# Optimization experiments

Hardware: AMD Instinct MI355X
Metric: run time of the kernel (lower is better)

Reference implementation:

```python
import jax, jax.numpy as jnp
import numpy as np

NEG_SLOPE = 0.01  # torch F.leaky_relu default
EPS = 1e-12


def setup_inputs() -> dict:
    key = jax.random.key(0)
    k1, k2, k3, k4 = jax.random.split(key, 4)
    num_nodes, in_f, out_f, num_edges = 50000, 128, 128, 600000
    x = jax.random.normal(k1, (num_nodes, in_f), dtype=jnp.float32)
    edge_index = jax.random.randint(k2, (2, num_edges), 0, num_nodes, dtype=jnp.int64)
    # xavier_uniform for W:[out,in]
    limit = float(np.sqrt(6.0 / (in_f + out_f)))
    W = jax.random.uniform(k3, (out_f, in_f), dtype=jnp.float32, minval=-limit, maxval=limit)
    a = jax.random.uniform(k4, (2 * out_f,), dtype=jnp.float32, minval=0.0, maxval=1.0)
    return {"x": x, "edge_index": edge_index, "W": W, "a": a}


def reference(x, edge_index, W, a):
    num_nodes = x.shape[0]
    out_f = W.shape[0]
    # add self loops
    loops = jnp.arange(num_nodes, dtype=edge_index.dtype)
    src = jnp.concatenate([edge_index[0], loops])
    dst = jnp.concatenate([edge_index[1], loops])
    messages = x @ W.T                      # [N, F_out]
    # cat([h_src,h_dst]) @ a == h_src @ a[:F] + h_dst @ a[F:] (avoids materializing concat)
    s_src = messages @ a[:out_f]            # [N]
    s_dst = messages @ a[out_f:]            # [N]
    e_ij = jax.nn.leaky_relu(s_src[src] + s_dst[dst], negative_slope=NEG_SLOPE)  # [E]
    w = jnp.exp(e_ij)                       # unnormalized edge weights
    denom = jax.ops.segment_sum(w, dst, num_segments=num_nodes)
    denom = jnp.maximum(denom, EPS)
    weighted = w[:, None] * messages[src]   # [E, F_out]
    agg = jax.ops.segment_sum(weighted, dst, num_segments=num_nodes)
    return agg / denom[:, None]
```

## Files before the change

### kernel.cpp

```cpp
#include <hip/hip_runtime.h>

#define NEG_SLOPE 0.01f
#define CH 4096
#define BSHIFT 9
#define BINW 512
#define NBMAX 128

typedef __attribute__((ext_vector_type(8))) short bf16x8;
typedef __attribute__((ext_vector_type(4))) float f32x4;

static __device__ __forceinline__ unsigned short f2bf(float f) {
  unsigned u = __float_as_uint(f);
  u += 0x7fffu + ((u >> 16) & 1u);
  return (unsigned short)(u >> 16);
}

__global__ __launch_bounds__(256) void k_setup(const float* __restrict__ W,
                                               const float* __restrict__ a,
                                               unsigned short* __restrict__ Wb,
                                               float* __restrict__ p_lo,
                                               float* __restrict__ p_hi,
                                               int* __restrict__ bin_cursor) {
  int b = blockIdx.x;
  int t = threadIdx.x;
  if (b < 64) {
    int i = b * 256 + t;
    Wb[i] = f2bf(W[i]);
    if (b == 0 && t < NBMAX) bin_cursor[t] = 0;
  } else {
    if (t < 128) {
      float lo = 0.f, hi = 0.f;
#pragma unroll 8
      for (int f = 0; f < 128; ++f) {
        float w = W[f * 128 + t];
        lo += w * a[f];
        hi += w * a[128 + f];
      }
      p_lo[t] = lo;
      p_hi[t] = hi;
    }
  }
}

__global__ __launch_bounds__(256) void k_work(const float* __restrict__ x,
                                              const float* __restrict__ p_lo,
                                              const float* __restrict__ p_hi,
                                              const unsigned short* __restrict__ Wb,
                                              unsigned short* __restrict__ msgs,
                                              float* __restrict__ s_src,
                                              float* __restrict__ s_dst, int N,
                                              const int* __restrict__ ei,
                                              int* __restrict__ bin_cursor,
                                              int2* __restrict__ binbuf, int E,
                                              int SB, int BINCAP) {
  __shared__ int hist[NBMAX], base[NBMAX], cur[NBMAX], gbase[NBMAX];
  __shared__ int2 stage[CH];
  int t = threadIdx.x;
  if ((int)blockIdx.x < SB) {
    int e0 = blockIdx.x * CH;
    int cntE = E - e0; if (cntE > CH) cntE = CH;
    if (t < NBMAX) { hist[t] = 0; cur[t] = 0; }
    __syncthreads();
    int srcs[CH / 256], dsts[CH / 256];
#pragma unroll
    for (int j = 0; j < CH / 256; ++j) {
      int i = t + j * 256;
      if (i < cntE) {
        srcs[j] = ei[e0 + i];
        dsts[j] = ei[E + e0 + i];
        atomicAdd(&hist[dsts[j] >> BSHIFT], 1);
      }
    }
    __syncthreads();
    if (t < NBMAX) base[t] = hist[t];
    __syncthreads();
    for (int d = 1; d < NBMAX; d <<= 1) {
      int v = (t < NBMAX && t >= d) ? base[t - d] : 0;
      __syncthreads();
      if (t < NBMAX) base[t] += v;
      __syncthreads();
    }
    if (t < NBMAX) {
      base[t] -= hist[t];
      gbase[t] = hist[t] ? atomicAdd(&bin_cursor[t], hist[t]) : 0;
    }
    __syncthreads();
#pragma unroll
    for (int j = 0; j < CH / 256; ++j) {
      int i = t + j * 256;
      if (i < cntE) {
        int bin = dsts[j] >> BSHIFT;
        int p = base[bin] + atomicAdd(&cur[bin], 1);
        stage[p] = make_int2(srcs[j], dsts[j]);
      }
    }
    __syncthreads();
    for (int i = t; i < cntE; i += 256) {
      int2 ed = stage[i];
      int bin = ed.y >> BSHIFT;
      int idx = gbase[bin] + (i - base[bin]);
      if (idx < BINCAP) binbuf[(size_t)bin * BINCAP + idx] = ed;
    }
    return;
  }
  int bb = blockIdx.x - SB;
  int wave = (bb * 256 + t) >> 6;
  int lane = t & 63;
  int baseN = wave * 16;
  if (baseN >= N) return;
  int q = lane >> 4, r = lane & 15;
  int node = baseN + r;
  const float* xrow = x + (size_t)node * 128 + q * 8;
  const float4* pl = (const float4*)p_lo;
  const float4* ph = (const float4*)p_hi;
  bf16x8 afrag[4];
  float lo = 0.f, hi = 0.f;
#pragma unroll
  for (int c = 0; c < 4; ++c) {
    float4 v0 = *(const float4*)(xrow + c * 32);
    float4 v1 = *(const float4*)(xrow + c * 32 + 4);
    int fi = q * 2 + c * 8;
    float4 a0 = pl[fi], a1 = pl[fi + 1];
    float4 b0 = ph[fi], b1 = ph[fi + 1];
    lo += v0.x * a0.x + v0.y * a0.y + v0.z * a0.z + v0.w * a0.w
        + v1.x * a1.x + v1.y * a1.y + v1.z * a1.z + v1.w * a1.w;
    hi += v0.x * b0.x + v0.y * b0.y + v0.z * b0.z + v0.w * b0.w
        + v1.x * b1.x + v1.y * b1.y + v1.z * b1.z + v1.w * b1.w;
    bf16x8 f;
    f[0] = (short)f2bf(v0.x); f[1] = (short)f2bf(v0.y);
    f[2] = (short)f2bf(v0.z); f[3] = (short)f2bf(v0.w);
    f[4] = (short)f2bf(v1.x); f[5] = (short)f2bf(v1.y);
    f[6] = (short)f2bf(v1.z); f[7] = (short)f2bf(v1.w);
    afrag[c] = f;
  }
  lo += __shfl_xor(lo, 16); lo += __shfl_xor(lo, 32);
  hi += __shfl_xor(hi, 16); hi += __shfl_xor(hi, 32);
  if (q == 0) { s_src[node] = lo; s_dst[node] = hi; }
#pragma unroll
  for (int ft = 0; ft < 8; ++ft) {
    const unsigned short* wrow = Wb + (size_t)(ft * 16 + r) * 128 + q * 8;
    f32x4 acc = {0.f, 0.f, 0.f, 0.f};
#pragma unroll
    for (int c = 0; c < 4; ++c) {
      bf16x8 bfrag = *(const bf16x8*)(wrow + c * 32);
      acc = __builtin_amdgcn_mfma_f32_16x16x32_bf16(afrag[c], bfrag, acc, 0, 0, 0);
    }
#pragma unroll
    for (int rr = 0; rr < 4; ++rr) {
      int n2 = baseN + q * 4 + rr;
      msgs[(size_t)n2 * 128 + ft * 16 + r] = f2bf(acc[rr]);
    }
  }
}

__global__ __launch_bounds__(256) void k_pass2(const int2* __restrict__ binbuf,
                                               const int* __restrict__ bin_cursor,
                                               unsigned* __restrict__ csr,
                                               int2* __restrict__ meta,
                                               int N, int BINCAP) {
  __shared__ int hist[BINW], scanv[BINW], cur[BINW];
  __shared__ int tmp[256];
  int b = blockIdx.x, t = threadIdx.x;
  int cnt = bin_cursor[b]; if (cnt > BINCAP) cnt = BINCAP;
  const int2* bb = binbuf + (size_t)b * BINCAP;
  hist[t] = 0; hist[t + 256] = 0;
  __syncthreads();
  for (int i = t; i < cnt; i += 256)
    atomicAdd(&hist[bb[i].y & (BINW - 1)], 1);
  __syncthreads();
  int v0 = hist[2 * t], v1 = hist[2 * t + 1];
  tmp[t] = v0 + v1;
  __syncthreads();
  for (int d = 1; d < 256; d <<= 1) {
    int v = (t >= d) ? tmp[t - d] : 0;
    __syncthreads();
    tmp[t] += v;
    __syncthreads();
  }
  int excl = tmp[t] - (v0 + v1);
  scanv[2 * t] = excl;
  scanv[2 * t + 1] = excl + v0;
  cur[2 * t] = 0; cur[2 * t + 1] = 0;
  __syncthreads();
  int gb = b * BINCAP;
  for (int l = t; l < BINW; l += 256) {
    int dst = b * BINW + l;
    if (dst < N) meta[dst] = make_int2(gb + scanv[l], hist[l]);
  }
  __syncthreads();
  for (int i = t; i < cnt; i += 256) {
    int2 ed = bb[i];
    int l = ed.y & (BINW - 1);
    int p = atomicAdd(&cur[l], 1);
    csr[gb + scanv[l] + p] = (unsigned)ed.x;
  }
}

__global__ __launch_bounds__(256) void k_agg(const unsigned short* __restrict__ msgs,
                                             const int2* __restrict__ meta,
                                             const unsigned* __restrict__ csr,
                                             const float* __restrict__ s_src,
                                             const float* __restrict__ s_dst,
                                             float* __restrict__ out, int N) {
  int wave = (blockIdx.x * 256 + threadIdx.x) >> 6;
  int lane = threadIdx.x & 63;
  if (wave >= N) return;
  int node = wave;
  int g = lane >> 4;
  int r = lane & 15;
  float sdn = s_dst[node];
  float zs = s_src[node] + sdn;
  zs = zs > 0.f ? zs : NEG_SLOPE * zs;
  float wself = expf(zs);
  float wg = (g == 0) ? wself : 0.f;
  float denom = wg;
  float acc[8];
  {
    const uint4* mrow = (const uint4*)(msgs + (size_t)node * 128);
    uint4 m = mrow[r];
    unsigned mm[4] = {m.x, m.y, m.z, m.w};
#pragma unroll
    for (int c = 0; c < 4; ++c) {
      acc[2 * c]     = wg * __uint_as_float(mm[c] << 16);
      acc[2 * c + 1] = wg * __uint_as_float(mm[c] & 0xffff0000u);
    }
  }
  int2 md = meta[node];
  int cnt = md.y;
  const unsigned* bucket = csr + md.x;
  int nIter = (cnt + 15) >> 4;
  for (int it = 0; it < nIter; ++it) {
    int kb = it * 16 + g;
    bool v[4];
    unsigned e[4];
    uint4 m[4];
    float ss[4];
#pragma unroll
    for (int u = 0; u < 4; ++u) {
      int k = kb + u * 4;
      v[u] = k < cnt;
      e[u] = bucket[v[u] ? k : 0];
    }
#pragma unroll
    for (int u = 0; u < 4; ++u)
      m[u] = ((const uint4*)(msgs + (size_t)e[u] * 128))[r];
#pragma unroll
    for (int u = 0; u < 4; ++u)
      ss[u] = s_src[e[u]];
#pragma unroll
    for (int u = 0; u < 4; ++u) {
      float z = ss[u] + sdn;
      z = z > 0.f ? z : NEG_SLOPE * z;
      float w = v[u] ? expf(z) : 0.f;
      unsigned mm[4] = {m[u].x, m[u].y, m[u].z, m[u].w};
#pragma unroll
      for (int c = 0; c < 4; ++c) {
        acc[2 * c]     += w * __uint_as_float(mm[c] << 16);
        acc[2 * c + 1] += w * __uint_as_float(mm[c] & 0xffff0000u);
      }
      denom += w;
    }
  }
#pragma unroll
  for (int mask = 16; mask < 64; mask <<= 1) {
#pragma unroll
    for (int j = 0; j < 8; ++j) acc[j] += __shfl_xor(acc[j], mask);
    denom += __shfl_xor(denom, mask);
  }
  if (g == 0) {
    float inv = 1.f / fmaxf(denom, 1e-12f);
    float4 o0 = {acc[0] * inv, acc[1] * inv, acc[2] * inv, acc[3] * inv};
    float4 o1 = {acc[4] * inv, acc[5] * inv, acc[6] * inv, acc[7] * inv};
    float4* orow = (float4*)(out + (size_t)node * 128);
    orow[r * 2] = o0;
    orow[r * 2 + 1] = o1;
  }
}

extern "C" void kernel_launch(void* const* d_in, const int* in_sizes, int n_in,
                              void* d_out, int out_size, void* d_ws, size_t ws_size,
                              hipStream_t stream) {
  const float* x = (const float*)d_in[0];
  const int* ei = (const int*)d_in[1];
  const float* W = (const float*)d_in[2];
  const float* a = (const float*)d_in[3];
  float* out = (float*)d_out;
  int N = in_sizes[0] / 128;
  int E = in_sizes[1] / 2;

  int NB = (N + BINW - 1) >> BSHIFT;
  int BINCAP = ((E / NB) + (E / NB) / 4 + 1024 + 255) & ~255;

  char* ws = (char*)d_ws;
  size_t off = 0;
  auto alloc = [&](size_t bytes) {
    off = (off + 255) & ~(size_t)255;
    void* p = ws + off;
    off += bytes;
    return p;
  };
  unsigned short* msgs = (unsigned short*)alloc((size_t)N * 128 * 2);
  float* s_src = (float*)alloc((size_t)N * 4);
  float* s_dst = (float*)alloc((size_t)N * 4);
  float* p_lo = (float*)alloc(512);
  float* p_hi = (float*)alloc(512);
  unsigned short* Wb = (unsigned short*)alloc(128 * 128 * 2);
  int* bin_cursor = (int*)alloc(NBMAX * 4);
  int2* binbuf = (int2*)alloc((size_t)NB * BINCAP * 8);
  unsigned* csr = (unsigned*)alloc((size_t)NB * BINCAP * 4);
  int2* meta = (int2*)alloc((size_t)N * 8);

  int waves = (N + 15) / 16;
  int SB = (E + CH - 1) / CH;
  int MB = (waves + 3) / 4;
  k_setup<<<65, 256, 0, stream>>>(W, a, Wb, p_lo, p_hi, bin_cursor);
  k_work<<<SB + MB, 256, 0, stream>>>(x, p_lo, p_hi, Wb, msgs, s_src, s_dst, N,
                                      ei, bin_cursor, binbuf, E, SB, BINCAP);
  k_pass2<<<NB, 256, 0, stream>>>(binbuf, bin_cursor, csr, meta, N, BINCAP);
  k_agg<<<(N + 3) / 4, 256, 0, stream>>>(msgs, meta, csr, s_src, s_dst, out, N);
}
```

Baseline: 147.8 us.

## Precompute edge attention weights during CSR build and store with source index

The edge weight exp(leaky_relu(s_src+s_dst)) is now computed in the binning pass and stored beside the source index in an int2 CSR entry. The aggregation kernel therefore no longer does a dependent gather of s_src or an exp per edge. The cost is a CSR twice as large, plus random s_src/s_dst reads in pass2. The edge chunk size is also halved to spread the binning work over more blocks.

```diff
diff --git a/kernel.cpp b/kernel.cpp
--- a/kernel.cpp
+++ b/kernel.cpp
@@ -1,7 +1,7 @@
 #include <hip/hip_runtime.h>
 
 #define NEG_SLOPE 0.01f
-#define CH 4096
+#define CH 2048
 #define BSHIFT 9
 #define BINW 512
 #define NBMAX 128
@@ -155,7 +155,9 @@
 
 __global__ __launch_bounds__(256) void k_pass2(const int2* __restrict__ binbuf,
                                                const int* __restrict__ bin_cursor,
-                                               unsigned* __restrict__ csr,
+                                               const float* __restrict__ s_src,
+                                               const float* __restrict__ s_dst,
+                                               int2* __restrict__ csr,
                                                int2* __restrict__ meta,
                                                int N, int BINCAP) {
   __shared__ int hist[BINW], scanv[BINW], cur[BINW];
@@ -190,15 +192,18 @@
   __syncthreads();
   for (int i = t; i < cnt; i += 256) {
     int2 ed = bb[i];
+    float z = s_src[ed.x] + s_dst[ed.y];
+    z = z > 0.f ? z : NEG_SLOPE * z;
+    float w = expf(z);
     int l = ed.y & (BINW - 1);
     int p = atomicAdd(&cur[l], 1);
-    csr[gb + scanv[l] + p] = (unsigned)ed.x;
+    csr[gb + scanv[l] + p] = make_int2(ed.x, __float_as_int(w));
   }
 }
 
 __global__ __launch_bounds__(256) void k_agg(const unsigned short* __restrict__ msgs,
                                              const int2* __restrict__ meta,
-                                             const unsigned* __restrict__ csr,
+                                             const int2* __restrict__ csr,
                                              const float* __restrict__ s_src,
                                              const float* __restrict__ s_dst,
                                              float* __restrict__ out, int N) {
@@ -208,8 +213,7 @@
   int node = wave;
   int g = lane >> 4;
   int r = lane & 15;
-  float sdn = s_dst[node];
-  float zs = s_src[node] + sdn;
+  float zs = s_src[node] + s_dst[node];
   zs = zs > 0.f ? zs : NEG_SLOPE * zs;
   float wself = expf(zs);
   float wg = (g == 0) ? wself : 0.f;
@@ -227,14 +231,13 @@
   }
   int2 md = meta[node];
   int cnt = md.y;
-  const unsigned* bucket = csr + md.x;
+  const int2* bucket = csr + md.x;
   int nIter = (cnt + 15) >> 4;
   for (int it = 0; it < nIter; ++it) {
     int kb = it * 16 + g;
     bool v[4];
-    unsigned e[4];
+    int2 e[4];
     uint4 m[4];
-    float ss[4];
 #pragma unroll
     for (int u = 0; u < 4; ++u) {
       int k = kb + u * 4;
@@ -243,15 +246,10 @@
     }
 #pragma unroll
     for (int u = 0; u < 4; ++u)
-      m[u] = ((const uint4*)(msgs + (size_t)e[u] * 128))[r];
-#pragma unroll
-    for (int u = 0; u < 4; ++u)
-      ss[u] = s_src[e[u]];
+      m[u] = ((const uint4*)(msgs + (size_t)e[u].x * 128))[r];
 #pragma unroll
     for (int u = 0; u < 4; ++u) {
-      float z = ss[u] + sdn;
-      z = z > 0.f ? z : NEG_SLOPE * z;
-      float w = v[u] ? expf(z) : 0.f;
+      float w = v[u] ? __int_as_float(e[u].y) : 0.f;
       unsigned mm[4] = {m[u].x, m[u].y, m[u].z, m[u].w};
 #pragma unroll
       for (int c = 0; c < 4; ++c) {
@@ -307,7 +305,7 @@
   unsigned short* Wb = (unsigned short*)alloc(128 * 128 * 2);
   int* bin_cursor = (int*)alloc(NBMAX * 4);
   int2* binbuf = (int2*)alloc((size_t)NB * BINCAP * 8);
-  unsigned* csr = (unsigned*)alloc((size_t)NB * BINCAP * 4);
+  int2* csr = (int2*)alloc((size_t)NB * BINCAP * 8);
   int2* meta = (int2*)alloc((size_t)N * 8);
 
   int waves = (N + 15) / 16;
@@ -316,6 +314,6 @@
   k_setup<<<65, 256, 0, stream>>>(W, a, Wb, p_lo, p_hi, bin_cursor);
   k_work<<<SB + MB, 256, 0, stream>>>(x, p_lo, p_hi, Wb, msgs, s_src, s_dst, N,
                                       ei, bin_cursor, binbuf, E, SB, BINCAP);
-  k_pass2<<<NB, 256, 0, stream>>>(binbuf, bin_cursor, csr, meta, N, BINCAP);
+  k_pass2<<<NB, 256, 0, stream>>>(binbuf, bin_cursor, s_src, s_dst, csr, meta, N, BINCAP);
   k_agg<<<(N + 3) / 4, 256, 0, stream>>>(msgs, meta, csr, s_src, s_dst, out, N);
 }
```

Result: slower. 155.3 us (+5.1%).
